# Performance work log

Hardware: AMD Instinct MI355X
Metric: run time of the kernel (lower is better)

## Reference

```python
import jax, jax.numpy as jnp
import numpy as np

N = 20000      # nodes
E = 50000      # edges
B = 128        # graphs in batch
H = 64         # hidden_dim
FEAT = 28      # raw node feature dim
N_TYPES = 100  # one-hot size for node_type
EDGE_DIM = 5   # one-hot size for edge_type
OUT = 1        # output_dim
MP_ITER = 3
S2S_ITER = 4


def setup_inputs() -> dict:
    key = jax.random.key(0)
    ks = jax.random.split(key, 24)
    s = 0.05
    inp = {
        'node_feat': jax.random.normal(ks[0], (N, FEAT), dtype=jnp.float32),
        'node_type': jax.random.randint(ks[1], (N,), 0, N_TYPES),
        'edge_index': jax.random.randint(ks[2], (2, E), 0, N),
        'edge_type': jax.random.randint(ks[3], (E,), 0, EDGE_DIM),
        'batch': jnp.sort(jax.random.randint(ks[4], (N,), 0, B)),
        # node embedding
        'W_emb': jax.random.normal(ks[5], (N_TYPES + FEAT, H), dtype=jnp.float32) * s,
        'b_emb': jnp.zeros((H,), dtype=jnp.float32),
        # shared edge net: edge_dim -> H -> H*H
        'W_e1': jax.random.normal(ks[6], (EDGE_DIM, H), dtype=jnp.float32) * s,
        'b_e1': jnp.zeros((H,), dtype=jnp.float32),
        'W_e2': jax.random.normal(ks[7], (H, H * H), dtype=jnp.float32) * s,
        'b_e2': jnp.zeros((H * H,), dtype=jnp.float32),
        # per-layer NNConv root weight + bias
        'roots': jax.random.normal(ks[8], (MP_ITER, H, H), dtype=jnp.float32) * s,
        'conv_bias': jnp.zeros((MP_ITER, H), dtype=jnp.float32),
        # Set2Set LSTM (input 2H, hidden H); torch gate order i,f,g,o
        'W_ih': jax.random.normal(ks[9], (4 * H, 2 * H), dtype=jnp.float32) * s,
        'W_hh': jax.random.normal(ks[10], (4 * H, H), dtype=jnp.float32) * s,
        'b_ih': jnp.zeros((4 * H,), dtype=jnp.float32),
        'b_hh': jnp.zeros((4 * H,), dtype=jnp.float32),
        # output MLP 2H -> H -> OUT
        'W_o1': jax.random.normal(ks[11], (2 * H, H), dtype=jnp.float32) * s,
        'b_o1': jnp.zeros((H,), dtype=jnp.float32),
        'W_o2': jax.random.normal(ks[12], (H, OUT), dtype=jnp.float32) * s,
        'b_o2': jnp.zeros((OUT,), dtype=jnp.float32),
    }
    return inp


def _forward(node_feat, W_emb, b_emb, W_e1, b_e1, W_e2, b_e2, roots, conv_bias,
             W_ih, W_hh, b_ih, b_hh, W_o1, b_o1, W_o2, b_o2,
             node_type, edge_index, edge_type, batch):
    # node embedding: [one_hot(node_type,100) ; node_feat] @ W_emb
    x_in = jnp.concatenate(
        [jax.nn.one_hot(node_type, N_TYPES, dtype=node_feat.dtype), node_feat], axis=-1)
    h = x_in @ W_emb + b_emb                                   # [N, H]

    # edge-conditioned weights (edge_attr is fixed, edge_net is shared across
    # iterations, so nn(edge_attr) is identical each layer -> compute once)
    edge_attr = jax.nn.one_hot(edge_type, EDGE_DIM, dtype=node_feat.dtype)
    Wmat = jax.nn.relu(edge_attr @ W_e1 + b_e1) @ W_e2 + b_e2  # [E, H*H]
    Wmat = Wmat.reshape(E, H, H)                               # [E, H_in, H_out]

    src, dst = edge_index[0], edge_index[1]
    for i in range(MP_ITER):
        msg = jnp.einsum('eh,eho->eo', h[src], Wmat)           # per-edge matvec
        agg = jax.ops.segment_sum(msg, dst, num_segments=N)    # sum aggregation
        h = agg + h @ roots[i] + conv_bias[i]                  # NNConv root + bias

    # Set2Set pooling
    hx = jnp.zeros((B, H), dtype=h.dtype)
    cx = jnp.zeros((B, H), dtype=h.dtype)
    q_star = jnp.zeros((B, 2 * H), dtype=h.dtype)
    for _ in range(S2S_ITER):
        gates = q_star @ W_ih.T + b_ih + hx @ W_hh.T + b_hh
        ig, fg, gg, og = jnp.split(gates, 4, axis=-1)
        cx = jax.nn.sigmoid(fg) * cx + jax.nn.sigmoid(ig) * jnp.tanh(gg)
        hx = jax.nn.sigmoid(og) * jnp.tanh(cx)
        q = hx                                                 # [B, H]
        e = jnp.sum(h * q[batch], axis=-1)                     # [N]
        m = jax.lax.stop_gradient(jax.ops.segment_max(e, batch, num_segments=B))
        a = jnp.exp(e - m[batch])
        denom = jax.ops.segment_sum(a, batch, num_segments=B)
        denom = jnp.where(denom == 0, 1.0, denom)
        a = a / denom[batch]                                   # scatter softmax
        r = jax.ops.segment_sum(a[:, None] * h, batch, num_segments=B)  # [B, H]
        q_star = jnp.concatenate([q, r], axis=-1)

    out = jax.nn.relu(q_star @ W_o1 + b_o1) @ W_o2 + b_o2      # [B, OUT]
    return out


def reference(node_feat, node_type, edge_index, edge_type, batch,
              W_emb, b_emb, W_e1, b_e1, W_e2, b_e2, roots, conv_bias,
              W_ih, W_hh, b_ih, b_hh, W_o1, b_o1, W_o2, b_o2):
    return _forward(node_feat, W_emb, b_emb, W_e1, b_e1, W_e2, b_e2, roots,
                    conv_bias, W_ih, W_hh, b_ih, b_hh, W_o1, b_o1, W_o2, b_o2,
                    node_type, edge_index, edge_type, batch)
```

## Files before the change

### kernel.cpp

```cpp
#include <hip/hip_runtime.h>
#include <math.h>


#define NN 20000
#define NE 50000
#define NB 128
#define HD 64
#define NFEAT 28
#define NTYPES 100
#define EDIM 5
#define MPIT 3
#define S2SIT 4
#define NBLK_E ((NE + 255) / 256)
#define SMAX 224
#define HP (HD + 1)

__device__ __forceinline__ float sigm(float x) {
  return 1.0f / (1.0f + expf(-x));
}

__global__ __launch_bounds__(256) void k_setup(
    const float* __restrict__ feat, const int* __restrict__ ntype,
    const int* __restrict__ etype, const int* __restrict__ batch,
    const float* __restrict__ W_emb, const float* __restrict__ b_emb,
    const float* __restrict__ W_e1, const float* __restrict__ b_e1,
    const float* __restrict__ W_e2, const float* __restrict__ b_e2,
    const float* __restrict__ W_ih, const float* __restrict__ W_hh,
    float* __restrict__ Wty, float* __restrict__ hA, float* __restrict__ hB,
    float* __restrict__ W_ihT, float* __restrict__ W_hhT,
    int* __restrict__ gstart, int* __restrict__ bc) {
  __shared__ float v[HD];
  __shared__ int wcc[4][EDIM];
  const int tid = threadIdx.x;
  const int lane = tid & 63;
  const int wv = tid >> 6;
  const int blk = blockIdx.x;
  const int nblk = gridDim.x;
  const int nthr = nblk << 8;
  const int gtid = (blk << 8) + tid;
  const int gw = (blk << 2) + wv;
  const int nwave = nblk << 2;

  if (blk < NBLK_E) {
    int e = (blk << 8) + tid;
    int ty = (e < NE) ? etype[e] : -1;
    #pragma unroll
    for (int t = 0; t < EDIM; ++t) {
      unsigned long long m = __ballot(ty == t);
      if (lane == 0) wcc[wv][t] = __popcll(m);
    }
    __syncthreads();
    if (tid < EDIM) {
      int s = wcc[0][tid] + wcc[1][tid] + wcc[2][tid] + wcc[3][tid];
      bc[blk * EDIM + tid] = s;
    }
    __syncthreads();
  }

  for (int u = blk; u < EDIM * 4; u += nblk) {
    int t = u >> 2, ch = u & 3;
    if (tid < HD) {
      float x = W_e1[t * HD + tid] + b_e1[tid];
      v[tid] = x > 0.f ? x : 0.f;
    }
    __syncthreads();
    #pragma unroll
    for (int i = 0; i < 4; ++i) {
      int m = ch * 1024 + i * 256 + tid;
      float acc = b_e2[m];
      #pragma unroll
      for (int j = 0; j < HD; ++j) acc = fmaf(v[j], W_e2[j * 4096 + m], acc);
      Wty[t * 4096 + m] = acc;
    }
    __syncthreads();
  }

  for (int o = gtid; o < 2 * HD * 4 * HD; o += nthr)
    W_ihT[o] = W_ih[(o & 255) * 128 + (o >> 8)];
  for (int o = gtid; o < HD * 4 * HD; o += nthr)
    W_hhT[o] = W_hh[(o & 255) * 64 + (o >> 8)];

  {
    float wf[NFEAT];
    #pragma unroll
    for (int f = 0; f < NFEAT; ++f) wf[f] = W_emb[(NTYPES + f) * HD + lane];
    float bb = b_emb[lane];
    for (int n = gw; n < NN; n += nwave) {
      int nu = __builtin_amdgcn_readfirstlane(n);
      int t = __builtin_amdgcn_readfirstlane(ntype[nu]);
      const float* row = feat + nu * NFEAT;
      float acc = bb + W_emb[t * HD + lane];
      #pragma unroll
      for (int f = 0; f < NFEAT; ++f) acc = fmaf(row[f], wf[f], acc);
      hA[nu * HD + lane] = acc;
    }
  }

  for (int n = gtid; n < NN; n += nthr) {
    int b = batch[n];
    if (n == 0)
      for (int t = 0; t <= b; ++t) gstart[t] = 0;
    int bn = (n + 1 < NN) ? batch[n + 1] : NB;
    for (int t = b + 1; t <= bn; ++t) gstart[t] = n + 1;
  }

  {
    float4 z = make_float4(0.f, 0.f, 0.f, 0.f);
    for (int i = gtid; i < NN * HD / 4; i += nthr)
      reinterpret_cast<float4*>(hB)[i] = z;
  }
}

__global__ __launch_bounds__(256) void k_place(
    const int* __restrict__ etype, const int* __restrict__ ei,
    const int* __restrict__ bc,
    int* __restrict__ srcs, int* __restrict__ dsts, int* __restrict__ offs_out) {
  __shared__ int s_base[EDIM];
  __shared__ int wc[4][EDIM];
  const int tid = threadIdx.x;
  const int lane = tid & 63;
  const int wv = tid >> 6;
  const int blk = blockIdx.x;

  if (wv == 0) {
    int part[EDIM], tot[EDIM];
    #pragma unroll
    for (int t = 0; t < EDIM; ++t) { part[t] = 0; tot[t] = 0; }
    for (int b = lane; b < NBLK_E; b += 64) {
      #pragma unroll
      for (int t = 0; t < EDIM; ++t) {
        int x = bc[b * EDIM + t];
        tot[t] += x;
        if (b < blk) part[t] += x;
      }
    }
    #pragma unroll
    for (int t = 0; t < EDIM; ++t) {
      #pragma unroll
      for (int off = 32; off; off >>= 1) {
        tot[t]  += __shfl_xor(tot[t],  off, 64);
        part[t] += __shfl_xor(part[t], off, 64);
      }
    }
    if (lane == 0) {
      int run = 0;
      #pragma unroll
      for (int t = 0; t < EDIM; ++t) {
        s_base[t] = run + part[t];
        if (blk == 0) offs_out[t] = run;
        run += tot[t];
      }
      if (blk == 0) offs_out[EDIM] = run;
    }
  }

  int e = (blk << 8) + tid;
  int ty = (e < NE) ? etype[e] : -1;
  int sv = 0, dv = 0;
  if (e < NE) { sv = ei[e]; dv = ei[NE + e]; }
  int rank = 0;
  #pragma unroll
  for (int t = 0; t < EDIM; ++t) {
    unsigned long long m = __ballot(ty == t);
    if (lane == 0) wc[wv][t] = __popcll(m);
    if (ty == t) rank = __popcll(m & ((1ull << lane) - 1ull));
  }
  __syncthreads();
  if (ty >= 0) {
    int base = s_base[ty];
    for (int w = 0; w < wv; ++w) base += wc[w][ty];
    srcs[base + rank] = sv;
    dsts[base + rank] = dv;
  }
}

__global__ __launch_bounds__(256) void k_mp(
    const int* __restrict__ srcs, const int* __restrict__ dsts,
    const int* __restrict__ offs_in,
    const float* __restrict__ Wty, const float* __restrict__ hsrc,
    float* __restrict__ htgt, float* __restrict__ hzero,
    const float* __restrict__ root, const float* __restrict__ bias) {
  const int lane = threadIdx.x & 63;
  const int wv = threadIdx.x >> 6;
  const int blk = blockIdx.x;

  if (blk < 512) {
    float w[HD];
    #pragma unroll
    for (int k = 0; k < HD; ++k) w[k] = root[k * HD + lane];
    float bb = bias[lane];
    int rw = (blk << 2) + wv;
    for (int n = rw; n < NN; n += 2048) {
      int nu = __builtin_amdgcn_readfirstlane(n);
      const float* row = hsrc + nu * HD;
      float a0 = bb, a1 = 0.f, a2 = 0.f, a3 = 0.f;
      #pragma unroll
      for (int k = 0; k < HD; k += 4) {
        a0 = fmaf(row[k + 0], w[k + 0], a0);
        a1 = fmaf(row[k + 1], w[k + 1], a1);
        a2 = fmaf(row[k + 2], w[k + 2], a2);
        a3 = fmaf(row[k + 3], w[k + 3], a3);
      }
      atomicAdd(&htgt[nu * HD + lane], (a0 + a1) + (a2 + a3));
    }
    if (hzero) {
      float4 z = make_float4(0.f, 0.f, 0.f, 0.f);
      for (int i = (blk << 8) + threadIdx.x; i < NN * HD / 4; i += 512 * 256)
        reinterpret_cast<float4*>(hzero)[i] = z;
    }
  } else {
    int wid = ((blk - 512) << 2) + wv;
    const int nw = 8192;
    int per = (NE + nw - 1) / nw;
    int beg = wid * per;
    int end = beg + per; if (end > NE) end = NE;
    if (beg >= end) return;
    int offs[EDIM + 1];
    #pragma unroll
    for (int t = 0; t <= EDIM; ++t) offs[t] = offs_in[t];
    for (int t = 0; t < EDIM; ++t) {
      int lo = offs[t];     if (lo < beg) lo = beg;
      int hi = offs[t + 1]; if (hi > end) hi = end;
      if (lo >= hi) continue;
      float w[HD];
      #pragma unroll
      for (int k = 0; k < HD; ++k) w[k] = Wty[t * 4096 + k * HD + lane];
      for (int p = lo; p < hi; ++p) {
        int s = __builtin_amdgcn_readfirstlane(srcs[p]);
        int d = __builtin_amdgcn_readfirstlane(dsts[p]);
        const float* row = hsrc + s * HD;
        float a0 = 0.f, a1 = 0.f, a2 = 0.f, a3 = 0.f;
        #pragma unroll
        for (int k = 0; k < HD; k += 4) {
          a0 = fmaf(row[k + 0], w[k + 0], a0);
          a1 = fmaf(row[k + 1], w[k + 1], a1);
          a2 = fmaf(row[k + 2], w[k + 2], a2);
          a3 = fmaf(row[k + 3], w[k + 3], a3);
        }
        atomicAdd(&htgt[d * HD + lane], (a0 + a1) + (a2 + a3));
      }
    }
  }
}

__global__ __launch_bounds__(256) void k_s2s(
    const float* __restrict__ h, const int* __restrict__ gstart,
    const float* __restrict__ W_ihT, const float* __restrict__ W_hhT,
    const float* __restrict__ b_ih, const float* __restrict__ b_hh,
    const float* __restrict__ W_o1, const float* __restrict__ b_o1,
    const float* __restrict__ W_o2, const float* __restrict__ b_o2,
    float* __restrict__ out) {
  __shared__ float hs[SMAX * HP];
  __shared__ float ebuf[SMAX];
  __shared__ float qstar[2 * HD];
  __shared__ float hxs[HD], cxs[HD], gates[4 * HD];
  __shared__ float redM[4], redS[4], redR[4][HD];
  __shared__ float hid[HD];
  int b = blockIdx.x;
  int tid = threadIdx.x;
  int lane = tid & 63, wv = tid >> 6;

  int st = gstart[b], en = gstart[b + 1];
  int cnt = en - st;
  int cached = cnt < SMAX ? cnt : SMAX;

  int total = cached * HD;
  for (int base = tid * 4; base < total; base += 1024) {
    float4 v = *reinterpret_cast<const float4*>(h + st * HD + base);
    int n = base >> 6, k = base & 63;
    float* row = hs + n * HP + k;
    row[0] = v.x; row[1] = v.y; row[2] = v.z; row[3] = v.w;
  }
  if (tid < 2 * HD) qstar[tid] = 0.f;
  if (tid < HD) { hxs[tid] = 0.f; cxs[tid] = 0.f; }
  __syncthreads();

  for (int it = 0; it < S2SIT; ++it) {
    float acc0 = b_ih[tid] + b_hh[tid], acc1 = 0.f;
    #pragma unroll 8
    for (int j = 0; j < 2 * HD; j += 2) {
      acc0 = fmaf(qstar[j],     W_ihT[j * 256 + tid],       acc0);
      acc1 = fmaf(qstar[j + 1], W_ihT[(j + 1) * 256 + tid], acc1);
    }
    #pragma unroll 8
    for (int j = 0; j < HD; j += 2) {
      acc0 = fmaf(hxs[j],     W_hhT[j * 256 + tid],       acc0);
      acc1 = fmaf(hxs[j + 1], W_hhT[(j + 1) * 256 + tid], acc1);
    }
    gates[tid] = acc0 + acc1;
    __syncthreads();
    if (tid < HD) {
      float ig = sigm(gates[tid]);
      float fg = sigm(gates[HD + tid]);
      float gg = tanhf(gates[2 * HD + tid]);
      float og = sigm(gates[3 * HD + tid]);
      float c = fmaf(fg, cxs[tid], ig * gg);
      cxs[tid] = c;
      hxs[tid] = og * tanhf(c);
    }
    __syncthreads();

    float e = -1e30f;
    if (tid < cached) {
      const float* row = hs + tid * HP;
      float d0 = 0.f, d1 = 0.f;
      #pragma unroll 8
      for (int k = 0; k < HD; k += 2) {
        d0 = fmaf(row[k],     hxs[k],     d0);
        d1 = fmaf(row[k + 1], hxs[k + 1], d1);
      }
      e = d0 + d1;
      ebuf[tid] = e;
    }
    float m = e;
    #pragma unroll
    for (int off = 32; off; off >>= 1) m = fmaxf(m, __shfl_xor(m, off, 64));
    float qreg = hxs[lane];
    for (int n = cached + wv; n < cnt; n += 4) {
      float ev = h[(st + n) * HD + lane] * qreg;
      #pragma unroll
      for (int off = 32; off; off >>= 1) ev += __shfl_xor(ev, off, 64);
      m = fmaxf(m, ev);
    }
    if (lane == 0) redM[wv] = m;
    __syncthreads();
    float M = fmaxf(fmaxf(redM[0], redM[1]), fmaxf(redM[2], redM[3]));

    float sp = 0.f;
    if (tid < cached) {
      float a = expf(ebuf[tid] - M);
      ebuf[tid] = a;
      sp = a;
    }
    #pragma unroll
    for (int off = 32; off; off >>= 1) sp += __shfl_xor(sp, off, 64);
    __syncthreads();

    float r = 0.f;
    for (int n = wv; n < cached; n += 4)
      r = fmaf(ebuf[n], hs[n * HP + lane], r);
    float s_tail = 0.f;
    for (int n = cached + wv; n < cnt; n += 4) {
      float v = h[(st + n) * HD + lane];
      float ev = v * qreg;
      #pragma unroll
      for (int off = 32; off; off >>= 1) ev += __shfl_xor(ev, off, 64);
      float a = expf(ev - M);
      s_tail += a;
      r = fmaf(a, v, r);
    }
    if (lane == 0) redS[wv] = sp + s_tail;
    redR[wv][lane] = r;
    __syncthreads();
    if (tid < HD) {
      float S = redS[0] + redS[1] + redS[2] + redS[3];
      float R = redR[0][tid] + redR[1][tid] + redR[2][tid] + redR[3][tid];
      if (S == 0.f) S = 1.f;
      qstar[tid] = hxs[tid];
      qstar[HD + tid] = R / S;
    }
    __syncthreads();
  }

  if (tid < HD) {
    float acc = b_o1[tid];
    #pragma unroll 8
    for (int i = 0; i < 2 * HD; ++i)
      acc = fmaf(qstar[i], W_o1[i * HD + tid], acc);
    hid[tid] = acc > 0.f ? acc : 0.f;
  }
  __syncthreads();
  if (tid < HD) {
    float p = hid[tid] * W_o2[tid];
    #pragma unroll
    for (int off = 32; off; off >>= 1) p += __shfl_xor(p, off, 64);
    if (tid == 0) out[b] = p + b_o2[0];
  }
}

extern "C" void kernel_launch(void* const* d_in, const int* in_sizes, int n_in,
                              void* d_out, int out_size, void* d_ws, size_t ws_size,
                              hipStream_t stream) {
  const float* node_feat = (const float*)d_in[0];
  const int*   node_type = (const int*)d_in[1];
  const int*   edge_index= (const int*)d_in[2];
  const int*   edge_type = (const int*)d_in[3];
  const int*   batch     = (const int*)d_in[4];
  const float* W_emb     = (const float*)d_in[5];
  const float* b_emb     = (const float*)d_in[6];
  const float* W_e1      = (const float*)d_in[7];
  const float* b_e1      = (const float*)d_in[8];
  const float* W_e2      = (const float*)d_in[9];
  const float* b_e2      = (const float*)d_in[10];
  const float* roots     = (const float*)d_in[11];
  const float* conv_bias = (const float*)d_in[12];
  const float* W_ih      = (const float*)d_in[13];
  const float* W_hh      = (const float*)d_in[14];
  const float* b_ih      = (const float*)d_in[15];
  const float* b_hh      = (const float*)d_in[16];
  const float* W_o1      = (const float*)d_in[17];
  const float* b_o1      = (const float*)d_in[18];
  const float* W_o2      = (const float*)d_in[19];
  const float* b_o2      = (const float*)d_in[20];
  float* out = (float*)d_out;

  float* Wty   = (float*)d_ws;
  float* hA    = Wty + EDIM * 4096;
  float* hB    = hA + NN * HD;
  float* hC    = hB + NN * HD;
  float* W_ihT = hC + NN * HD;
  float* W_hhT = W_ihT + 2 * HD * 4 * HD;
  int*   srcs  = (int*)(W_hhT + HD * 4 * HD);
  int*   dsts  = srcs + NE;
  int*   gstart= dsts + NE;
  int*   bc    = gstart + 136;
  int*   offs  = bc + NBLK_E * EDIM;

  k_setup<<<512, 256, 0, stream>>>(node_feat, node_type, edge_type, batch,
                                   W_emb, b_emb, W_e1, b_e1, W_e2, b_e2,
                                   W_ih, W_hh, Wty, hA, hB, W_ihT, W_hhT,
                                   gstart, bc);
  k_place<<<NBLK_E, 256, 0, stream>>>(edge_type, edge_index, bc, srcs, dsts, offs);

  k_mp<<<2560, 256, 0, stream>>>(srcs, dsts, offs, Wty, hA, hB, hC,
                                 roots + 0 * HD * HD, conv_bias + 0 * HD);
  k_mp<<<2560, 256, 0, stream>>>(srcs, dsts, offs, Wty, hB, hC, hA,
                                 roots + 1 * HD * HD, conv_bias + 1 * HD);
  k_mp<<<2560, 256, 0, stream>>>(srcs, dsts, offs, Wty, hC, hA, (float*)0,
                                 roots + 2 * HD * HD, conv_bias + 2 * HD);

  k_s2s<<<NB, 256, 0, stream>>>(hA, gstart, W_ihT, W_hhT, b_ih, b_hh,
                                W_o1, b_o1, W_o2, b_o2, out);
}
```

Baseline: 251.2 us.

## Replace atomic scatter with CSR-by-destination two-phase message passing

Message passing now builds a destination-sorted CSR (per-node degree counts, a single-block scan, per-edge slot positions). Each edge message is written to its own slot, and a second kernel gathers each node's messages together with the root transform, so the float atomicAdds and the per-layer buffer zeroing go away. The node embedding moves into its own kernel. In exchange this adds three setup kernels, including a serial single-block scan, doubles the message-passing launches, and adds a 50000x64 message buffer round trip through memory per layer.

```diff
diff --git a/kernel.cpp b/kernel.cpp
--- a/kernel.cpp
+++ b/kernel.cpp
@@ -19,16 +19,14 @@
   return 1.0f / (1.0f + expf(-x));
 }
 
-__global__ __launch_bounds__(256) void k_setup(
-    const float* __restrict__ feat, const int* __restrict__ ntype,
+__global__ __launch_bounds__(256) void k_prep(
     const int* __restrict__ etype, const int* __restrict__ batch,
-    const float* __restrict__ W_emb, const float* __restrict__ b_emb,
     const float* __restrict__ W_e1, const float* __restrict__ b_e1,
     const float* __restrict__ W_e2, const float* __restrict__ b_e2,
     const float* __restrict__ W_ih, const float* __restrict__ W_hh,
-    float* __restrict__ Wty, float* __restrict__ hA, float* __restrict__ hB,
-    float* __restrict__ W_ihT, float* __restrict__ W_hhT,
-    int* __restrict__ gstart, int* __restrict__ bc) {
+    float* __restrict__ Wty, float* __restrict__ W_ihT, float* __restrict__ W_hhT,
+    int* __restrict__ gstart, int* __restrict__ bc,
+    int* __restrict__ dcnt, int* __restrict__ dcur) {
   __shared__ float v[HD];
   __shared__ int wcc[4][EDIM];
   const int tid = threadIdx.x;
@@ -38,8 +36,6 @@
   const int nblk = gridDim.x;
   const int nthr = nblk << 8;
   const int gtid = (blk << 8) + tid;
-  const int gw = (blk << 2) + wv;
-  const int nwave = nblk << 2;
 
   if (blk < NBLK_E) {
     int e = (blk << 8) + tid;
@@ -50,10 +46,8 @@
       if (lane == 0) wcc[wv][t] = __popcll(m);
     }
     __syncthreads();
-    if (tid < EDIM) {
-      int s = wcc[0][tid] + wcc[1][tid] + wcc[2][tid] + wcc[3][tid];
-      bc[blk * EDIM + tid] = s;
-    }
+    if (tid < EDIM)
+      bc[blk * EDIM + tid] = wcc[0][tid] + wcc[1][tid] + wcc[2][tid] + wcc[3][tid];
     __syncthreads();
   }
 
@@ -79,22 +73,6 @@
     W_ihT[o] = W_ih[(o & 255) * 128 + (o >> 8)];
   for (int o = gtid; o < HD * 4 * HD; o += nthr)
     W_hhT[o] = W_hh[(o & 255) * 64 + (o >> 8)];
-
-  {
-    float wf[NFEAT];
-    #pragma unroll
-    for (int f = 0; f < NFEAT; ++f) wf[f] = W_emb[(NTYPES + f) * HD + lane];
-    float bb = b_emb[lane];
-    for (int n = gw; n < NN; n += nwave) {
-      int nu = __builtin_amdgcn_readfirstlane(n);
-      int t = __builtin_amdgcn_readfirstlane(ntype[nu]);
-      const float* row = feat + nu * NFEAT;
-      float acc = bb + W_emb[t * HD + lane];
-      #pragma unroll
-      for (int f = 0; f < NFEAT; ++f) acc = fmaf(row[f], wf[f], acc);
-      hA[nu * HD + lane] = acc;
-    }
-  }
 
   for (int n = gtid; n < NN; n += nthr) {
     int b = batch[n];
@@ -104,17 +82,36 @@
     for (int t = b + 1; t <= bn; ++t) gstart[t] = n + 1;
   }
 
-  {
-    float4 z = make_float4(0.f, 0.f, 0.f, 0.f);
-    for (int i = gtid; i < NN * HD / 4; i += nthr)
-      reinterpret_cast<float4*>(hB)[i] = z;
+  for (int i = gtid; i < NN; i += nthr) { dcnt[i] = 0; dcur[i] = 0; }
+}
+
+__global__ __launch_bounds__(256) void k_embed(
+    const float* __restrict__ feat, const int* __restrict__ ntype,
+    const float* __restrict__ W_emb, const float* __restrict__ b_emb,
+    float* __restrict__ h) {
+  const int lane = threadIdx.x & 63;
+  const int gw = (blockIdx.x << 2) + (threadIdx.x >> 6);
+  const int nwave = gridDim.x << 2;
+  float wf[NFEAT];
+  #pragma unroll
+  for (int f = 0; f < NFEAT; ++f) wf[f] = W_emb[(NTYPES + f) * HD + lane];
+  float bb = b_emb[lane];
+  for (int n = gw; n < NN; n += nwave) {
+    int nu = __builtin_amdgcn_readfirstlane(n);
+    int t = __builtin_amdgcn_readfirstlane(ntype[nu]);
+    const float* row = feat + nu * NFEAT;
+    float acc = bb + W_emb[t * HD + lane];
+    #pragma unroll
+    for (int f = 0; f < NFEAT; ++f) acc = fmaf(row[f], wf[f], acc);
+    h[nu * HD + lane] = acc;
   }
 }
 
 __global__ __launch_bounds__(256) void k_place(
     const int* __restrict__ etype, const int* __restrict__ ei,
     const int* __restrict__ bc,
-    int* __restrict__ srcs, int* __restrict__ dsts, int* __restrict__ offs_out) {
+    int* __restrict__ srcs, int* __restrict__ dsts, int* __restrict__ offs_out,
+    int* __restrict__ dcnt) {
   __shared__ int s_base[EDIM];
   __shared__ int wc[4][EDIM];
   const int tid = threadIdx.x;
@@ -171,29 +168,75 @@
     for (int w = 0; w < wv; ++w) base += wc[w][ty];
     srcs[base + rank] = sv;
     dsts[base + rank] = dv;
-  }
-}
-
-__global__ __launch_bounds__(256) void k_mp(
-    const int* __restrict__ srcs, const int* __restrict__ dsts,
-    const int* __restrict__ offs_in,
-    const float* __restrict__ Wty, const float* __restrict__ hsrc,
-    float* __restrict__ htgt, float* __restrict__ hzero,
-    const float* __restrict__ root, const float* __restrict__ bias) {
+    atomicAdd(&dcnt[dv], 1);
+  }
+}
+
+__global__ __launch_bounds__(256) void k_dscan(
+    const int* __restrict__ dcnt, int* __restrict__ dstart) {
+  __shared__ int buf[256];
+  const int tid = threadIdx.x;
+  const int CH = (NN + 255) / 256;
+  int base = tid * CH;
+  int s = 0;
+  for (int i = 0; i < CH; ++i) {
+    int n = base + i;
+    if (n < NN) s += dcnt[n];
+  }
+  buf[tid] = s;
+  __syncthreads();
+  #pragma unroll
+  for (int off = 1; off < 256; off <<= 1) {
+    int x = (tid >= off) ? buf[tid - off] : 0;
+    __syncthreads();
+    buf[tid] += x;
+    __syncthreads();
+  }
+  int run = buf[tid] - s;
+  for (int i = 0; i < CH; ++i) {
+    int n = base + i;
+    if (n < NN) { dstart[n] = run; run += dcnt[n]; }
+  }
+  if (tid == 255) dstart[NN] = run;
+}
+
+__global__ __launch_bounds__(256) void k_dpos(
+    const int* __restrict__ dsts, const int* __restrict__ dstart,
+    int* __restrict__ dcur, int* __restrict__ dpos) {
+  int p = (blockIdx.x << 8) + threadIdx.x;
+  if (p >= NE) return;
+  int d = dsts[p];
+  int r = atomicAdd(&dcur[d], 1);
+  dpos[p] = dstart[d] + r;
+}
+
+__global__ __launch_bounds__(256) void k_mpA(
+    const int* __restrict__ srcs, const int* __restrict__ dpos,
+    const int* __restrict__ offs_in, const float* __restrict__ Wty,
+    const float* __restrict__ hsrc, float* __restrict__ msg) {
   const int lane = threadIdx.x & 63;
   const int wv = threadIdx.x >> 6;
-  const int blk = blockIdx.x;
-
-  if (blk < 512) {
+  int wid = (blockIdx.x << 2) + wv;
+  const int nw = 8192;
+  int per = (NE + nw - 1) / nw;
+  int beg = wid * per;
+  int end = beg + per; if (end > NE) end = NE;
+  if (beg >= end) return;
+  int offs[EDIM + 1];
+  #pragma unroll
+  for (int t = 0; t <= EDIM; ++t) offs[t] = offs_in[t];
+  for (int t = 0; t < EDIM; ++t) {
+    int lo = offs[t];     if (lo < beg) lo = beg;
+    int hi = offs[t + 1]; if (hi > end) hi = end;
+    if (lo >= hi) continue;
     float w[HD];
     #pragma unroll
-    for (int k = 0; k < HD; ++k) w[k] = root[k * HD + lane];
-    float bb = bias[lane];
-    int rw = (blk << 2) + wv;
-    for (int n = rw; n < NN; n += 2048) {
-      int nu = __builtin_amdgcn_readfirstlane(n);
-      const float* row = hsrc + nu * HD;
-      float a0 = bb, a1 = 0.f, a2 = 0.f, a3 = 0.f;
+    for (int k = 0; k < HD; ++k) w[k] = Wty[t * 4096 + k * HD + lane];
+    for (int p = lo; p < hi; ++p) {
+      int s = __builtin_amdgcn_readfirstlane(srcs[p]);
+      int dp = __builtin_amdgcn_readfirstlane(dpos[p]);
+      const float* row = hsrc + s * HD;
+      float a0 = 0.f, a1 = 0.f, a2 = 0.f, a3 = 0.f;
       #pragma unroll
       for (int k = 0; k < HD; k += 4) {
         a0 = fmaf(row[k + 0], w[k + 0], a0);
@@ -201,45 +244,39 @@
         a2 = fmaf(row[k + 2], w[k + 2], a2);
         a3 = fmaf(row[k + 3], w[k + 3], a3);
       }
-      atomicAdd(&htgt[nu * HD + lane], (a0 + a1) + (a2 + a3));
-    }
-    if (hzero) {
-      float4 z = make_float4(0.f, 0.f, 0.f, 0.f);
-      for (int i = (blk << 8) + threadIdx.x; i < NN * HD / 4; i += 512 * 256)
-        reinterpret_cast<float4*>(hzero)[i] = z;
-    }
-  } else {
-    int wid = ((blk - 512) << 2) + wv;
-    const int nw = 8192;
-    int per = (NE + nw - 1) / nw;
-    int beg = wid * per;
-    int end = beg + per; if (end > NE) end = NE;
-    if (beg >= end) return;
-    int offs[EDIM + 1];
-    #pragma unroll
-    for (int t = 0; t <= EDIM; ++t) offs[t] = offs_in[t];
-    for (int t = 0; t < EDIM; ++t) {
-      int lo = offs[t];     if (lo < beg) lo = beg;
-      int hi = offs[t + 1]; if (hi > end) hi = end;
-      if (lo >= hi) continue;
-      float w[HD];
-      #pragma unroll
-      for (int k = 0; k < HD; ++k) w[k] = Wty[t * 4096 + k * HD + lane];
-      for (int p = lo; p < hi; ++p) {
-        int s = __builtin_amdgcn_readfirstlane(srcs[p]);
-        int d = __builtin_amdgcn_readfirstlane(dsts[p]);
-        const float* row = hsrc + s * HD;
-        float a0 = 0.f, a1 = 0.f, a2 = 0.f, a3 = 0.f;
-        #pragma unroll
-        for (int k = 0; k < HD; k += 4) {
-          a0 = fmaf(row[k + 0], w[k + 0], a0);
-          a1 = fmaf(row[k + 1], w[k + 1], a1);
-          a2 = fmaf(row[k + 2], w[k + 2], a2);
-          a3 = fmaf(row[k + 3], w[k + 3], a3);
-        }
-        atomicAdd(&htgt[d * HD + lane], (a0 + a1) + (a2 + a3));
-      }
-    }
+      msg[dp * HD + lane] = (a0 + a1) + (a2 + a3);
+    }
+  }
+}
+
+__global__ __launch_bounds__(256) void k_mpB(
+    const int* __restrict__ dstart, const float* __restrict__ msg,
+    const float* __restrict__ hsrc, const float* __restrict__ root,
+    const float* __restrict__ bias, float* __restrict__ htgt) {
+  const int lane = threadIdx.x & 63;
+  const int gw = (blockIdx.x << 2) + (threadIdx.x >> 6);
+  const int nwave = gridDim.x << 2;
+  float w[HD];
+  #pragma unroll
+  for (int k = 0; k < HD; ++k) w[k] = root[k * HD + lane];
+  float bb = bias[lane];
+  for (int n = gw; n < NN; n += nwave) {
+    int nu = __builtin_amdgcn_readfirstlane(n);
+    float rowv = hsrc[nu * HD + lane];
+    float acc = bb;
+    #pragma unroll
+    for (int k = 0; k < HD; ++k)
+      acc = fmaf(__shfl(rowv, k, 64), w[k], acc);
+    int st = __builtin_amdgcn_readfirstlane(dstart[nu]);
+    int en = __builtin_amdgcn_readfirstlane(dstart[nu + 1]);
+    int j = st;
+    for (; j + 1 < en; j += 2) {
+      float a = msg[j * HD + lane];
+      float b = msg[(j + 1) * HD + lane];
+      acc += a + b;
+    }
+    if (j < en) acc += msg[j * HD + lane];
+    htgt[nu * HD + lane] = acc;
   }
 }
 
@@ -408,26 +445,37 @@
   float* hA    = Wty + EDIM * 4096;
   float* hB    = hA + NN * HD;
   float* hC    = hB + NN * HD;
-  float* W_ihT = hC + NN * HD;
+  float* msg   = hC + NN * HD;
+  float* W_ihT = msg + NE * HD;
   float* W_hhT = W_ihT + 2 * HD * 4 * HD;
   int*   srcs  = (int*)(W_hhT + HD * 4 * HD);
   int*   dsts  = srcs + NE;
-  int*   gstart= dsts + NE;
+  int*   dpos  = dsts + NE;
+  int*   gstart= dpos + NE;
   int*   bc    = gstart + 136;
   int*   offs  = bc + NBLK_E * EDIM;
-
-  k_setup<<<512, 256, 0, stream>>>(node_feat, node_type, edge_type, batch,
-                                   W_emb, b_emb, W_e1, b_e1, W_e2, b_e2,
-                                   W_ih, W_hh, Wty, hA, hB, W_ihT, W_hhT,
-                                   gstart, bc);
-  k_place<<<NBLK_E, 256, 0, stream>>>(edge_type, edge_index, bc, srcs, dsts, offs);
-
-  k_mp<<<2560, 256, 0, stream>>>(srcs, dsts, offs, Wty, hA, hB, hC,
-                                 roots + 0 * HD * HD, conv_bias + 0 * HD);
-  k_mp<<<2560, 256, 0, stream>>>(srcs, dsts, offs, Wty, hB, hC, hA,
-                                 roots + 1 * HD * HD, conv_bias + 1 * HD);
-  k_mp<<<2560, 256, 0, stream>>>(srcs, dsts, offs, Wty, hC, hA, (float*)0,
-                                 roots + 2 * HD * HD, conv_bias + 2 * HD);
+  int*   dcnt  = offs + 8;
+  int*   dcur  = dcnt + NN;
+  int*   dstart= dcur + NN;
+
+  k_prep<<<256, 256, 0, stream>>>(edge_type, batch, W_e1, b_e1, W_e2, b_e2,
+                                  W_ih, W_hh, Wty, W_ihT, W_hhT, gstart, bc,
+                                  dcnt, dcur);
+  k_embed<<<1250, 256, 0, stream>>>(node_feat, node_type, W_emb, b_emb, hA);
+  k_place<<<NBLK_E, 256, 0, stream>>>(edge_type, edge_index, bc, srcs, dsts,
+                                      offs, dcnt);
+  k_dscan<<<1, 256, 0, stream>>>(dcnt, dstart);
+  k_dpos<<<NBLK_E, 256, 0, stream>>>(dsts, dstart, dcur, dpos);
+
+  k_mpA<<<2048, 256, 0, stream>>>(srcs, dpos, offs, Wty, hA, msg);
+  k_mpB<<<1250, 256, 0, stream>>>(dstart, msg, hA, roots + 0 * HD * HD,
+                                  conv_bias + 0 * HD, hB);
+  k_mpA<<<2048, 256, 0, stream>>>(srcs, dpos, offs, Wty, hB, msg);
+  k_mpB<<<1250, 256, 0, stream>>>(dstart, msg, hB, roots + 1 * HD * HD,
+                                  conv_bias + 1 * HD, hC);
+  k_mpA<<<2048, 256, 0, stream>>>(srcs, dpos, offs, Wty, hC, msg);
+  k_mpB<<<1250, 256, 0, stream>>>(dstart, msg, hC, roots + 2 * HD * HD,
+                                  conv_bias + 2 * HD, hA);
 
   k_s2s<<<NB, 256, 0, stream>>>(hA, gstart, W_ihT, W_hhT, b_ih, b_hh,
                                 W_o1, b_o1, W_o2, b_o2, out);
```

Measured after the change: 350.2 us. +39.4%, slower.
